# Kernel tuning notes

Measured on AMD Instinct MI355X. Metric: run time of the kernel, lower is better.

## Reference

```python
import jax, jax.numpy as jnp
import numpy as np

N, D, P, Q = 4096, 512, 8, 32
MARGIN = 1.0
L2_WEIGHT = 0.005
EPS = 1e-6  # torch.nn.PairwiseDistance default eps, added to the difference


def setup_inputs() -> dict:
    key = jax.random.key(0)
    k1, k2, k3 = jax.random.split(key, 3)
    batch = jax.random.normal(k1, (N, D), dtype=jnp.float32)
    anchors = jnp.arange(N, dtype=jnp.int64) if jax.config.jax_enable_x64 else jnp.arange(N, dtype=jnp.int32)
    pos_idx = jax.random.randint(k2, (N, P), 0, N)
    neg_idx = jax.random.randint(k3, (N, Q), 0, N)
    return {"batch": batch, "anchors": anchors, "pos_idx": pos_idx, "neg_idx": neg_idx}


def reference(batch, anchors, pos_idx, neg_idx):
    # batch: [N, D]; anchors: [N]; pos_idx: [N, P]; neg_idx: [N, Q]
    a = batch[anchors]                       # [N, D]
    # PairwiseDistance(p=2): (sum |x - y + eps|^2)^(1/2)
    d_pos = jnp.sqrt(jnp.sum((a[:, None, :] - batch[pos_idx] + EPS) ** 2, axis=-1))  # [N, P]
    d_neg = jnp.sqrt(jnp.sum((a[:, None, :] - batch[neg_idx] + EPS) ** 2, axis=-1))  # [N, Q]
    pos_term = jax.scipy.special.logsumexp(d_pos, axis=1)            # [N]
    neg_term = jax.scipy.special.logsumexp(MARGIN - d_neg, axis=1)   # [N]
    per_anchor = jax.nn.relu(pos_term + neg_term)                    # [N]
    l2_term = L2_WEIGHT * jnp.mean(jnp.sqrt(jnp.sum(batch ** 2, axis=1)))
    return jnp.mean(per_anchor) + l2_term
```

## Files before the change

kernel.cpp:

```cpp
#include <hip/hip_runtime.h>
#include <math.h>
#include <float.h>

#define NN 4096
#define DD 512
#define PP 8
#define QQ 32
#define NB_TOT 40
#define NPW 5
constexpr float MARGIN = 1.0f;
constexpr float L2W    = 0.005f;
constexpr float EPS    = 1e-6f;

__device__ inline float wave_reduce_sum(float v) {
    v += __shfl_xor(v, 32, 64);
    v += __shfl_xor(v, 16, 64);
    v += __shfl_xor(v,  8, 64);
    v += __shfl_xor(v,  4, 64);
    v += __shfl_xor(v,  2, 64);
    v += __shfl_xor(v,  1, 64);
    return v;
}

__device__ inline float wave_reduce_max(float v) {
    v = fmaxf(v, __shfl_xor(v, 32, 64));
    v = fmaxf(v, __shfl_xor(v, 16, 64));
    v = fmaxf(v, __shfl_xor(v,  8, 64));
    v = fmaxf(v, __shfl_xor(v,  4, 64));
    v = fmaxf(v, __shfl_xor(v,  2, 64));
    v = fmaxf(v, __shfl_xor(v,  1, 64));
    return v;
}

__global__ __launch_bounds__(512) void dist_kernel(
    const float* __restrict__ batch,
    const int*   __restrict__ anchors,
    const int*   __restrict__ pos_idx,
    const int*   __restrict__ neg_idx,
    float*       __restrict__ ws)
{
    const int i    = blockIdx.x;
    const int tid  = threadIdx.x;
    const int lane = tid & 63;
    const int wave = tid >> 6;
    const int jb   = wave * NPW;

    __shared__ float dist[NB_TOT];
    __shared__ float norm_sh;

    const int arow = anchors[i];
    const float* __restrict__ ap = batch + (size_t)arow * DD + lane * 8;
    float4 a0 = *reinterpret_cast<const float4*>(ap);
    float4 a1 = *reinterpret_cast<const float4*>(ap + 4);
    a0.x += EPS; a0.y += EPS; a0.z += EPS; a0.w += EPS;
    a1.x += EPS; a1.y += EPS; a1.z += EPS; a1.w += EPS;

    if (wave == 7) {
        const float* __restrict__ rp = batch + (size_t)i * DD + lane * 8;
        const float4 r0 = *reinterpret_cast<const float4*>(rp);
        const float4 r1 = *reinterpret_cast<const float4*>(rp + 4);
        float s = r0.x*r0.x + r0.y*r0.y + r0.z*r0.z + r0.w*r0.w
                + r1.x*r1.x + r1.y*r1.y + r1.z*r1.z + r1.w*r1.w;
        s = wave_reduce_sum(s);
        if (lane == 0) norm_sh = sqrtf(s);
    }

    int idxs[NPW];
    #pragma unroll
    for (int t = 0; t < NPW; ++t) {
        const int j = jb + t;
        idxs[t] = (j < PP) ? pos_idx[i * PP + j] : neg_idx[i * QQ + (j - PP)];
    }

    float4 b0[NPW], b1[NPW];
    #pragma unroll
    for (int t = 0; t < NPW; ++t) {
        const float* __restrict__ bp = batch + (size_t)idxs[t] * DD + lane * 8;
        b0[t] = *reinterpret_cast<const float4*>(bp);
        b1[t] = *reinterpret_cast<const float4*>(bp + 4);
    }

    float s[NPW];
    #pragma unroll
    for (int t = 0; t < NPW; ++t) {
        float d, acc = 0.0f;
        d = a0.x - b0[t].x; acc = fmaf(d, d, acc);
        d = a0.y - b0[t].y; acc = fmaf(d, d, acc);
        d = a0.z - b0[t].z; acc = fmaf(d, d, acc);
        d = a0.w - b0[t].w; acc = fmaf(d, d, acc);
        d = a1.x - b1[t].x; acc = fmaf(d, d, acc);
        d = a1.y - b1[t].y; acc = fmaf(d, d, acc);
        d = a1.z - b1[t].z; acc = fmaf(d, d, acc);
        d = a1.w - b1[t].w; acc = fmaf(d, d, acc);
        s[t] = acc;
    }

    #pragma unroll
    for (int t = 0; t < NPW; ++t) s[t] = wave_reduce_sum(s[t]);

    float v = s[0];
    v = (lane == 1) ? s[1] : v;
    v = (lane == 2) ? s[2] : v;
    v = (lane == 3) ? s[3] : v;
    v = (lane == 4) ? s[4] : v;
    if (lane < NPW) dist[jb + lane] = sqrtf(v);

    __syncthreads();

    if (wave == 0) {
        const float d = (lane < NB_TOT) ? dist[lane] : 0.0f;

        const bool pact = (lane < PP);
        const float pm = wave_reduce_max(pact ? d : -FLT_MAX);
        const float ps = wave_reduce_sum(pact ? expf(d - pm) : 0.0f);
        const float pos_term = pm + logf(ps);

        const bool nact = (lane >= PP) && (lane < NB_TOT);
        const float nv = MARGIN - d;
        const float nm = wave_reduce_max(nact ? nv : -FLT_MAX);
        const float ns = wave_reduce_sum(nact ? expf(nv - nm) : 0.0f);
        const float neg_term = nm + logf(ns);

        if (lane == 0)
            ws[i] = fmaxf(0.0f, pos_term + neg_term) + L2W * norm_sh;
    }
}

__global__ __launch_bounds__(256) void reduce_kernel(
    const float* __restrict__ ws, float* __restrict__ out)
{
    const int tid  = threadIdx.x;
    const int lane = tid & 63;
    const int wave = tid >> 6;

    const float4* __restrict__ w4 = reinterpret_cast<const float4*>(ws);
    float s = 0.0f;
    #pragma unroll
    for (int k = 0; k < 4; ++k) {
        const float4 v = w4[tid + 256 * k];
        s += v.x + v.y + v.z + v.w;
    }
    s = wave_reduce_sum(s);

    __shared__ float part[4];
    if (lane == 0) part[wave] = s;
    __syncthreads();
    if (tid == 0)
        out[0] = (part[0] + part[1] + part[2] + part[3]) * (1.0f / (float)NN);
}

extern "C" void kernel_launch(void* const* d_in, const int* in_sizes, int n_in,
                              void* d_out, int out_size, void* d_ws, size_t ws_size,
                              hipStream_t stream) {
    const float* batch   = (const float*)d_in[0];
    const int*   anchors = (const int*)d_in[1];
    const int*   pos_idx = (const int*)d_in[2];
    const int*   neg_idx = (const int*)d_in[3];
    float*       ws      = (float*)d_ws;
    float*       out     = (float*)d_out;

    dist_kernel<<<NN, 512, 0, stream>>>(batch, anchors, pos_idx, neg_idx, ws);
    reduce_kernel<<<1, 256, 0, stream>>>(ws, out);
}
```

Measured before the change: 91.35 us.

## Split feature dimension into two halves processed in separate cache-friendly passes

Repacks the batch into two contiguous half-width copies (low and high 256 columns) and runs the gather-distance kernel twice, once per half. Each pass gathers from a 4 MB array instead of 8 MB, so the working set can fit in L2/LLC and random row gathers hit cache more often. Partial squared distances and norms go to workspace between passes, and the final reduction kernel is replaced by a scaled atomicAdd into the output. The cost is an extra full copy of the batch, an extra launch, workspace round trips, and an order-dependent float atomic sum.

New measurement: 138.5 us. 1.52x slower.

```diff
diff --git a/kernel.cpp b/kernel.cpp
--- a/kernel.cpp
+++ b/kernel.cpp
@@ -4,6 +4,8 @@
 
 #define NN 4096
 #define DD 512
+#define HD 256
+#define HF4 64
 #define PP 8
 #define QQ 32
 #define NB_TOT 40
@@ -11,6 +13,11 @@
 constexpr float MARGIN = 1.0f;
 constexpr float L2W    = 0.005f;
 constexpr float EPS    = 1e-6f;
+
+#define WS_LO 0
+#define WS_HI (NN * HD)
+#define WS_D  (2 * NN * HD)
+#define WS_N  (WS_D + NN * NB_TOT)
 
 __device__ inline float wave_reduce_sum(float v) {
     v += __shfl_xor(v, 32, 64);
@@ -32,12 +39,30 @@
     return v;
 }
 
-__global__ __launch_bounds__(512) void dist_kernel(
-    const float* __restrict__ batch,
-    const int*   __restrict__ anchors,
-    const int*   __restrict__ pos_idx,
-    const int*   __restrict__ neg_idx,
-    float*       __restrict__ ws)
+__global__ __launch_bounds__(256) void repack_kernel(
+    const float4* __restrict__ batch4,
+    float4* __restrict__ lo4,
+    float4* __restrict__ hi4,
+    float*  __restrict__ out)
+{
+    const int t   = blockIdx.x * 256 + threadIdx.x;
+    const int row = t >> 7;
+    const int c   = t & 127;
+    const float4 v = batch4[t];
+    if (c < HF4) lo4[row * HF4 + c]         = v;
+    else         hi4[row * HF4 + (c - HF4)] = v;
+    if (t == 0) out[0] = 0.0f;
+}
+
+template<bool FIN>
+__global__ __launch_bounds__(512) void phase_kernel(
+    const float4* __restrict__ half4,
+    const int*    __restrict__ anchors,
+    const int*    __restrict__ pos_idx,
+    const int*    __restrict__ neg_idx,
+    float*        __restrict__ wsD,
+    float*        __restrict__ wsN,
+    float*        __restrict__ out)
 {
     const int i    = blockIdx.x;
     const int tid  = threadIdx.x;
@@ -49,21 +74,19 @@
     __shared__ float norm_sh;
 
     const int arow = anchors[i];
-    const float* __restrict__ ap = batch + (size_t)arow * DD + lane * 8;
-    float4 a0 = *reinterpret_cast<const float4*>(ap);
-    float4 a1 = *reinterpret_cast<const float4*>(ap + 4);
-    a0.x += EPS; a0.y += EPS; a0.z += EPS; a0.w += EPS;
-    a1.x += EPS; a1.y += EPS; a1.z += EPS; a1.w += EPS;
+    float4 a = half4[(size_t)arow * HF4 + lane];
 
     if (wave == 7) {
-        const float* __restrict__ rp = batch + (size_t)i * DD + lane * 8;
-        const float4 r0 = *reinterpret_cast<const float4*>(rp);
-        const float4 r1 = *reinterpret_cast<const float4*>(rp + 4);
-        float s = r0.x*r0.x + r0.y*r0.y + r0.z*r0.z + r0.w*r0.w
-                + r1.x*r1.x + r1.y*r1.y + r1.z*r1.z + r1.w*r1.w;
+        const float4 r = half4[(size_t)i * HF4 + lane];
+        float s = r.x*r.x + r.y*r.y + r.z*r.z + r.w*r.w;
         s = wave_reduce_sum(s);
-        if (lane == 0) norm_sh = sqrtf(s);
+        if (lane == 0) {
+            if (FIN) norm_sh = sqrtf(s + wsN[i]);
+            else     wsN[i]  = s;
+        }
     }
+
+    a.x += EPS; a.y += EPS; a.z += EPS; a.w += EPS;
 
     int idxs[NPW];
     #pragma unroll
@@ -72,26 +95,19 @@
         idxs[t] = (j < PP) ? pos_idx[i * PP + j] : neg_idx[i * QQ + (j - PP)];
     }
 
-    float4 b0[NPW], b1[NPW];
+    float4 b[NPW];
     #pragma unroll
-    for (int t = 0; t < NPW; ++t) {
-        const float* __restrict__ bp = batch + (size_t)idxs[t] * DD + lane * 8;
-        b0[t] = *reinterpret_cast<const float4*>(bp);
-        b1[t] = *reinterpret_cast<const float4*>(bp + 4);
-    }
+    for (int t = 0; t < NPW; ++t)
+        b[t] = half4[(size_t)idxs[t] * HF4 + lane];
 
     float s[NPW];
     #pragma unroll
     for (int t = 0; t < NPW; ++t) {
         float d, acc = 0.0f;
-        d = a0.x - b0[t].x; acc = fmaf(d, d, acc);
-        d = a0.y - b0[t].y; acc = fmaf(d, d, acc);
-        d = a0.z - b0[t].z; acc = fmaf(d, d, acc);
-        d = a0.w - b0[t].w; acc = fmaf(d, d, acc);
-        d = a1.x - b1[t].x; acc = fmaf(d, d, acc);
-        d = a1.y - b1[t].y; acc = fmaf(d, d, acc);
-        d = a1.z - b1[t].z; acc = fmaf(d, d, acc);
-        d = a1.w - b1[t].w; acc = fmaf(d, d, acc);
+        d = a.x - b[t].x; acc = fmaf(d, d, acc);
+        d = a.y - b[t].y; acc = fmaf(d, d, acc);
+        d = a.z - b[t].z; acc = fmaf(d, d, acc);
+        d = a.w - b[t].w; acc = fmaf(d, d, acc);
         s[t] = acc;
     }
 
@@ -103,7 +119,14 @@
     v = (lane == 2) ? s[2] : v;
     v = (lane == 3) ? s[3] : v;
     v = (lane == 4) ? s[4] : v;
-    if (lane < NPW) dist[jb + lane] = sqrtf(v);
+
+    if (!FIN) {
+        if (lane < NPW) wsD[i * NB_TOT + jb + lane] = v;
+        return;
+    }
+
+    if (lane < NPW)
+        dist[jb + lane] = sqrtf(v + wsD[i * NB_TOT + jb + lane]);
 
     __syncthreads();
 
@@ -121,44 +144,32 @@
         const float ns = wave_reduce_sum(nact ? expf(nv - nm) : 0.0f);
         const float neg_term = nm + logf(ns);
 
-        if (lane == 0)
-            ws[i] = fmaxf(0.0f, pos_term + neg_term) + L2W * norm_sh;
+        if (lane == 0) {
+            const float val = fmaxf(0.0f, pos_term + neg_term) + L2W * norm_sh;
+            atomicAdd(out, val * (1.0f / (float)NN));
+        }
     }
-}
-
-__global__ __launch_bounds__(256) void reduce_kernel(
-    const float* __restrict__ ws, float* __restrict__ out)
-{
-    const int tid  = threadIdx.x;
-    const int lane = tid & 63;
-    const int wave = tid >> 6;
-
-    const float4* __restrict__ w4 = reinterpret_cast<const float4*>(ws);
-    float s = 0.0f;
-    #pragma unroll
-    for (int k = 0; k < 4; ++k) {
-        const float4 v = w4[tid + 256 * k];
-        s += v.x + v.y + v.z + v.w;
-    }
-    s = wave_reduce_sum(s);
-
-    __shared__ float part[4];
-    if (lane == 0) part[wave] = s;
-    __syncthreads();
-    if (tid == 0)
-        out[0] = (part[0] + part[1] + part[2] + part[3]) * (1.0f / (float)NN);
 }
 
 extern "C" void kernel_launch(void* const* d_in, const int* in_sizes, int n_in,
                               void* d_out, int out_size, void* d_ws, size_t ws_size,
                               hipStream_t stream) {
-    const float* batch   = (const float*)d_in[0];
-    const int*   anchors = (const int*)d_in[1];
-    const int*   pos_idx = (const int*)d_in[2];
-    const int*   neg_idx = (const int*)d_in[3];
-    float*       ws      = (float*)d_ws;
-    float*       out     = (float*)d_out;
+    const float*  batch   = (const float*)d_in[0];
+    const int*    anchors = (const int*)d_in[1];
+    const int*    pos_idx = (const int*)d_in[2];
+    const int*    neg_idx = (const int*)d_in[3];
+    float*        wsf     = (float*)d_ws;
+    float*        out     = (float*)d_out;
 
-    dist_kernel<<<NN, 512, 0, stream>>>(batch, anchors, pos_idx, neg_idx, ws);
-    reduce_kernel<<<1, 256, 0, stream>>>(ws, out);
+    const float4* batch4 = (const float4*)batch;
+    float4*       lo4    = (float4*)(wsf + WS_LO);
+    float4*       hi4    = (float4*)(wsf + WS_HI);
+    float*        wsD    = wsf + WS_D;
+    float*        wsN    = wsf + WS_N;
+
+    repack_kernel<<<2048, 256, 0, stream>>>(batch4, lo4, hi4, out);
+    phase_kernel<false><<<NN, 512, 0, stream>>>(lo4, anchors, pos_idx, neg_idx,
+                                                wsD, wsN, out);
+    phase_kernel<true ><<<NN, 512, 0, stream>>>(hi4, anchors, pos_idx, neg_idx,
+                                                wsD, wsN, out);
 }
```

## Pre-convert batch to fp16 and gather half rows in distance kernel

Applied to the files above, without the earlier changes.

A new pre-pass converts the fp32 batch to fp16 in workspace and computes the row norms there. The distance kernel then gathers the anchor and the 40 neighbour rows at half the bytes, with 4 waves each handling 10 neighbours instead of 8 waves handling 5. This targets the random-gather memory traffic, which dominates. In exchange it adds a full conversion pass over the batch plus a third kernel launch, and fp16 rounding changes the distances slightly; the EPS of 1e-6 is now added after rounding the anchor.

Result: faster. 85.11 us (-6.8%).

```diff
diff --git a/kernel.cpp b/kernel.cpp
--- a/kernel.cpp
+++ b/kernel.cpp
@@ -7,10 +7,15 @@
 #define PP 8
 #define QQ 32
 #define NB_TOT 40
-#define NPW 5
+#define NPW 10
 constexpr float MARGIN = 1.0f;
 constexpr float L2W    = 0.005f;
 constexpr float EPS    = 1e-6f;
+
+typedef _Float16 half8 __attribute__((ext_vector_type(8)));
+
+#define WS_NORM (NN * DD / 2)
+#define WS_RES  (WS_NORM + NN)
 
 __device__ inline float wave_reduce_sum(float v) {
     v += __shfl_xor(v, 32, 64);
@@ -32,12 +37,37 @@
     return v;
 }
 
-__global__ __launch_bounds__(512) void dist_kernel(
-    const float* __restrict__ batch,
+__global__ __launch_bounds__(256) void convert_kernel(
+    const float4* __restrict__ batch4,
+    half8*        __restrict__ hb,
+    float*        __restrict__ norms)
+{
+    const int row  = blockIdx.x * 4 + (threadIdx.x >> 6);
+    const int lane = threadIdx.x & 63;
+
+    const float4 v0 = batch4[row * 128 + lane * 2];
+    const float4 v1 = batch4[row * 128 + lane * 2 + 1];
+
+    half8 h;
+    h[0] = (_Float16)v0.x; h[1] = (_Float16)v0.y;
+    h[2] = (_Float16)v0.z; h[3] = (_Float16)v0.w;
+    h[4] = (_Float16)v1.x; h[5] = (_Float16)v1.y;
+    h[6] = (_Float16)v1.z; h[7] = (_Float16)v1.w;
+    hb[row * 64 + lane] = h;
+
+    float s = v0.x*v0.x + v0.y*v0.y + v0.z*v0.z + v0.w*v0.w
+            + v1.x*v1.x + v1.y*v1.y + v1.z*v1.z + v1.w*v1.w;
+    s = wave_reduce_sum(s);
+    if (lane == 0) norms[row] = sqrtf(s);
+}
+
+__global__ __launch_bounds__(256) void dist_kernel(
+    const half8* __restrict__ hb,
     const int*   __restrict__ anchors,
     const int*   __restrict__ pos_idx,
     const int*   __restrict__ neg_idx,
-    float*       __restrict__ ws)
+    const float* __restrict__ norms,
+    float*       __restrict__ res)
 {
     const int i    = blockIdx.x;
     const int tid  = threadIdx.x;
@@ -46,24 +76,12 @@
     const int jb   = wave * NPW;
 
     __shared__ float dist[NB_TOT];
-    __shared__ float norm_sh;
 
     const int arow = anchors[i];
-    const float* __restrict__ ap = batch + (size_t)arow * DD + lane * 8;
-    float4 a0 = *reinterpret_cast<const float4*>(ap);
-    float4 a1 = *reinterpret_cast<const float4*>(ap + 4);
-    a0.x += EPS; a0.y += EPS; a0.z += EPS; a0.w += EPS;
-    a1.x += EPS; a1.y += EPS; a1.z += EPS; a1.w += EPS;
-
-    if (wave == 7) {
-        const float* __restrict__ rp = batch + (size_t)i * DD + lane * 8;
-        const float4 r0 = *reinterpret_cast<const float4*>(rp);
-        const float4 r1 = *reinterpret_cast<const float4*>(rp + 4);
-        float s = r0.x*r0.x + r0.y*r0.y + r0.z*r0.z + r0.w*r0.w
-                + r1.x*r1.x + r1.y*r1.y + r1.z*r1.z + r1.w*r1.w;
-        s = wave_reduce_sum(s);
-        if (lane == 0) norm_sh = sqrtf(s);
-    }
+    const half8 ah = hb[(size_t)arow * 64 + lane];
+    float a[8];
+    #pragma unroll
+    for (int k = 0; k < 8; ++k) a[k] = (float)ah[k] + EPS;
 
     int idxs[NPW];
     #pragma unroll
@@ -72,26 +90,20 @@
         idxs[t] = (j < PP) ? pos_idx[i * PP + j] : neg_idx[i * QQ + (j - PP)];
     }
 
-    float4 b0[NPW], b1[NPW];
+    half8 bh[NPW];
     #pragma unroll
-    for (int t = 0; t < NPW; ++t) {
-        const float* __restrict__ bp = batch + (size_t)idxs[t] * DD + lane * 8;
-        b0[t] = *reinterpret_cast<const float4*>(bp);
-        b1[t] = *reinterpret_cast<const float4*>(bp + 4);
-    }
+    for (int t = 0; t < NPW; ++t)
+        bh[t] = hb[(size_t)idxs[t] * 64 + lane];
 
     float s[NPW];
     #pragma unroll
     for (int t = 0; t < NPW; ++t) {
-        float d, acc = 0.0f;
-        d = a0.x - b0[t].x; acc = fmaf(d, d, acc);
-        d = a0.y - b0[t].y; acc = fmaf(d, d, acc);
-        d = a0.z - b0[t].z; acc = fmaf(d, d, acc);
-        d = a0.w - b0[t].w; acc = fmaf(d, d, acc);
-        d = a1.x - b1[t].x; acc = fmaf(d, d, acc);
-        d = a1.y - b1[t].y; acc = fmaf(d, d, acc);
-        d = a1.z - b1[t].z; acc = fmaf(d, d, acc);
-        d = a1.w - b1[t].w; acc = fmaf(d, d, acc);
+        float acc = 0.0f;
+        #pragma unroll
+        for (int k = 0; k < 8; ++k) {
+            const float d = a[k] - (float)bh[t][k];
+            acc = fmaf(d, d, acc);
+        }
         s[t] = acc;
     }
 
@@ -99,10 +111,8 @@
     for (int t = 0; t < NPW; ++t) s[t] = wave_reduce_sum(s[t]);
 
     float v = s[0];
-    v = (lane == 1) ? s[1] : v;
-    v = (lane == 2) ? s[2] : v;
-    v = (lane == 3) ? s[3] : v;
-    v = (lane == 4) ? s[4] : v;
+    #pragma unroll
+    for (int t = 1; t < NPW; ++t) v = (lane == t) ? s[t] : v;
     if (lane < NPW) dist[jb + lane] = sqrtf(v);
 
     __syncthreads();
@@ -122,18 +132,18 @@
         const float neg_term = nm + logf(ns);
 
         if (lane == 0)
-            ws[i] = fmaxf(0.0f, pos_term + neg_term) + L2W * norm_sh;
+            res[i] = fmaxf(0.0f, pos_term + neg_term) + L2W * norms[i];
     }
 }
 
 __global__ __launch_bounds__(256) void reduce_kernel(
-    const float* __restrict__ ws, float* __restrict__ out)
+    const float* __restrict__ res, float* __restrict__ out)
 {
     const int tid  = threadIdx.x;
     const int lane = tid & 63;
     const int wave = tid >> 6;
 
-    const float4* __restrict__ w4 = reinterpret_cast<const float4*>(ws);
+    const float4* __restrict__ w4 = reinterpret_cast<const float4*>(res);
     float s = 0.0f;
     #pragma unroll
     for (int k = 0; k < 4; ++k) {
@@ -156,9 +166,14 @@
     const int*   anchors = (const int*)d_in[1];
     const int*   pos_idx = (const int*)d_in[2];
     const int*   neg_idx = (const int*)d_in[3];
-    float*       ws      = (float*)d_ws;
+    float*       wsf     = (float*)d_ws;
     float*       out     = (float*)d_out;
 
-    dist_kernel<<<NN, 512, 0, stream>>>(batch, anchors, pos_idx, neg_idx, ws);
-    reduce_kernel<<<1, 256, 0, stream>>>(ws, out);
+    half8* hb    = (half8*)wsf;
+    float* norms = wsf + WS_NORM;
+    float* res   = wsf + WS_RES;
+
+    convert_kernel<<<NN / 4, 256, 0, stream>>>((const float4*)batch, hb, norms);
+    dist_kernel<<<NN, 256, 0, stream>>>(hb, anchors, pos_idx, neg_idx, norms, res);
+    reduce_kernel<<<1, 256, 0, stream>>>(res, out);
 }
```
